# Optimization experiments

Measured on AMD Instinct MI355X. Metric: run time of the kernel, lower is better.

The kernel has to match this reference:

```python
import jax, jax.numpy as jnp
import numpy as np

N_NODES = 50000
N_EDGES = 1600000
NUM_GRAPHS = 512
HID = 128
EDGE_DIM = 64
N_CONV = 4
BN_EPS = 1e-5


def setup_inputs() -> dict:
    key = jax.random.key(0)
    ks = jax.random.split(key, 16)
    x = jax.random.normal(ks[0], (N_NODES, 9), dtype=jnp.float32)
    edge_index = jax.random.randint(ks[1], (2, N_EDGES), 0, N_NODES, dtype=jnp.int64)
    edge_attr = jax.random.normal(ks[2], (N_EDGES, EDGE_DIM), dtype=jnp.float32)
    batch = jnp.sort(jax.random.randint(ks[3], (N_NODES,), 0, NUM_GRAPHS, dtype=jnp.int64))
    s = 0.05
    W_emb = jax.random.normal(ks[4], (9, HID), dtype=jnp.float32) * s
    b_emb = jnp.zeros((HID,), jnp.float32)
    zin = 2 * HID + EDGE_DIM  # 320: cat([x_i, x_j, edge_attr])
    Wf = jax.random.normal(ks[5], (N_CONV, zin, HID), dtype=jnp.float32) * s
    bf = jnp.zeros((N_CONV, HID), jnp.float32)
    Ws = jax.random.normal(ks[6], (N_CONV, zin, HID), dtype=jnp.float32) * s
    bs = jnp.zeros((N_CONV, HID), jnp.float32)
    gamma = jnp.ones((N_CONV, HID), jnp.float32)
    beta = jnp.zeros((N_CONV, HID), jnp.float32)
    W1 = jax.random.normal(ks[7], (HID, HID // 2), dtype=jnp.float32) * s
    b1 = jnp.zeros((HID // 2,), jnp.float32)
    W2 = jax.random.normal(ks[8], (HID // 2, 1), dtype=jnp.float32) * s
    b2 = jnp.zeros((1,), jnp.float32)
    return dict(x=x, edge_index=edge_index, edge_attr=edge_attr, batch=batch,
                W_emb=W_emb, b_emb=b_emb, Wf=Wf, bf=bf, Ws=Ws, bs=bs,
                gamma=gamma, beta=beta, W1=W1, b1=b1, W2=W2, b2=b2)


def _segment_mean(vals, idx, num_segments):
    s = jax.ops.segment_sum(vals, idx, num_segments=num_segments)
    cnt = jax.ops.segment_sum(jnp.ones((vals.shape[0], 1), vals.dtype), idx,
                              num_segments=num_segments)
    return s / jnp.maximum(cnt, 1.0)


def _forward(x, edge_index, edge_attr, batch, W_emb, b_emb, Wf, bf, Ws, bs,
             gamma, beta, W1, b1, W2, b2):
    src, dst = edge_index[0], edge_index[1]  # x_j = x[src], x_i = x[dst]
    h = x @ W_emb + b_emb  # [N, HID]
    for l in range(N_CONV):
        residual = h
        # lin(cat([x_i, x_j, e])) == x_i@W[:H] + x_j@W[H:2H] + e@W[2H:] + b,
        # with node projections done at N granularity before the edge gather.
        f = (h @ Wf[l, :HID])[dst] + (h @ Wf[l, HID:2 * HID])[src] \
            + edge_attr @ Wf[l, 2 * HID:] + bf[l]
        g = (h @ Ws[l, :HID])[dst] + (h @ Ws[l, HID:2 * HID])[src] \
            + edge_attr @ Ws[l, 2 * HID:] + bs[l]
        msg = jax.nn.sigmoid(f) * jax.nn.softplus(g)  # [E, HID]
        aggr = _segment_mean(msg, dst, N_NODES)
        h_conv = aggr + h  # CGConv internal residual
        # BatchNorm1d (training-mode batch stats, biased variance)
        mu = jnp.mean(h_conv, axis=0)
        var = jnp.mean(jnp.square(h_conv - mu), axis=0)
        h_bn = gamma[l] * (h_conv - mu) * jax.lax.rsqrt(var + BN_EPS) + beta[l]
        h = jax.nn.relu(h_bn) + residual  # dropout = identity (eval)
    pooled = _segment_mean(h, batch, NUM_GRAPHS)  # [G, HID]
    out = jax.nn.softplus(pooled @ W1 + b1) @ W2 + b2
    return out.squeeze(-1)  # [G]


def reference(x, edge_index, edge_attr, batch, W_emb, b_emb, Wf, bf, Ws, bs,
              gamma, beta, W1, b1, W2, b2):
    return _forward(x, edge_index, edge_attr, batch, W_emb, b_emb, Wf, bf,
                    Ws, bs, gamma, beta, W1, b1, W2, b2)
```

## Files before the change

kernel.cpp:

```cpp
#include <hip/hip_runtime.h>
#include <math.h>

#define N_NODES 50000
#define N_EDGES 1600000
#define NGRAPH  512
#define HID     128
#define EDIM    64
#define NCONV   4
#define MAXWI   150064
#define NPAD    (N_NODES + 32)
#define EGRID   2560

typedef __attribute__((ext_vector_type(8))) short short8;
typedef __attribute__((ext_vector_type(4))) float f32x4;
typedef unsigned int  u32;
typedef unsigned short u16;

#define MFMA16(a, b, c) __builtin_amdgcn_mfma_f32_16x16x32_bf16(a, b, c, 0, 0, 0)

__device__ __forceinline__ float fsig(float x) {
  return __builtin_amdgcn_rcpf(1.f + __expf(-x));
}
__device__ __forceinline__ float fsp(float x) {
  return fmaxf(x, 0.f) + __logf(1.f + __expf(-fabsf(x)));
}
__device__ __forceinline__ u16 f2bf(float x) {
  u32 u = __float_as_uint(x);
  return (u16)((u + 0x7fff + ((u >> 16) & 1)) >> 16);
}
__device__ __forceinline__ u32 f2bf_pack(float lo, float hi) {
  u32 a = __float_as_uint(lo), b = __float_as_uint(hi);
  u32 ra = (a + 0x7fff + ((a >> 16) & 1)) >> 16;
  u32 rb = (b + 0x7fff + ((b >> 16) & 1)) & 0xffff0000u;
  return ra | rb;
}
__device__ __forceinline__ short8 cvt8(float4 a, float4 b) {
  union { short8 s; u32 u[4]; } r;
  r.u[0] = f2bf_pack(a.x, a.y);
  r.u[1] = f2bf_pack(a.z, a.w);
  r.u[2] = f2bf_pack(b.x, b.y);
  r.u[3] = f2bf_pack(b.z, b.w);
  return r.s;
}

__global__ __launch_bounds__(256) void k_embed(const float* __restrict__ x,
                                               const float* __restrict__ Wemb,
                                               const float* __restrict__ bemb,
                                               float* __restrict__ h,
                                               u16* __restrict__ hb, u16* __restrict__ hlo) {
  int i = blockIdx.x * blockDim.x + threadIdx.x;
  if (i >= N_NODES * HID) return;
  int n = i >> 7, c = i & 127;
  const float* xr = x + (size_t)n * 9;
  float acc = bemb[c];
#pragma unroll
  for (int k = 0; k < 9; k++) acc = fmaf(xr[k], Wemb[k * HID + c], acc);
  h[i] = acc;
  u16 hi16 = f2bf(acc);
  hb[i] = hi16;
  hlo[i] = f2bf(acc - __uint_as_float((u32)hi16 << 16));
}

__global__ __launch_bounds__(256) void k_count(const int* __restrict__ ei, int* __restrict__ cnt) {
  int e = blockIdx.x * blockDim.x + threadIdx.x;
  if (e >= N_EDGES) return;
  atomicAdd(&cnt[ei[N_EDGES + e]], 1);
}

__global__ __launch_bounds__(256) void k_scan1(const int* __restrict__ cnt, int* __restrict__ bsum) {
  __shared__ int s[256];
  int i = blockIdx.x * 256 + threadIdx.x;
  s[threadIdx.x] = (i < N_NODES) ? cnt[i] : 0;
  __syncthreads();
  for (int o = 128; o > 0; o >>= 1) {
    if (threadIdx.x < o) s[threadIdx.x] += s[threadIdx.x + o];
    __syncthreads();
  }
  if (threadIdx.x == 0) bsum[blockIdx.x] = s[0];
}

__global__ __launch_bounds__(256) void k_scan2(int* __restrict__ bsum, int nb) {
  __shared__ int s[256];
  int tid = threadIdx.x;
  s[tid] = (tid < nb) ? bsum[tid] : 0;
  __syncthreads();
  for (int o = 1; o < 256; o <<= 1) {
    int t = (tid >= o) ? s[tid - o] : 0;
    __syncthreads();
    s[tid] += t;
    __syncthreads();
  }
  if (tid < nb) bsum[tid] = (tid == 0) ? 0 : s[tid - 1];
}

__global__ __launch_bounds__(256) void k_scan3(const int* __restrict__ cnt, const int* __restrict__ bsum,
                                               int* __restrict__ row_start, float* __restrict__ inv) {
  __shared__ int s[256];
  int i = blockIdx.x * 256 + threadIdx.x;
  int v = (i < N_NODES) ? cnt[i] : 0;
  s[threadIdx.x] = v;
  __syncthreads();
  for (int o = 1; o < 256; o <<= 1) {
    int t = (threadIdx.x >= o) ? s[threadIdx.x - o] : 0;
    __syncthreads();
    s[threadIdx.x] += t;
    __syncthreads();
  }
  if (i < N_NODES) {
    row_start[i + 1] = s[threadIdx.x] + bsum[blockIdx.x];
    inv[i] = 1.0f / (float)max(v, 1);
    if (i == 0) row_start[0] = 0;
  }
}

__global__ __launch_bounds__(256) void k_fill(const int* __restrict__ ei, const int* __restrict__ row_start,
                                              int* __restrict__ cur, int* __restrict__ eids,
                                              int* __restrict__ esrc) {
  int e = blockIdx.x * blockDim.x + threadIdx.x;
  if (e < 64) {
    eids[N_EDGES + e] = 0;
    esrc[N_EDGES + e] = 0;
  }
  if (e >= N_EDGES) return;
  int s = ei[e], d = ei[N_EDGES + e];
  int pos = row_start[d] + atomicAdd(&cur[d], 1);
  eids[pos] = e;
  esrc[pos] = s;
}

__global__ __launch_bounds__(256) void k_tilecnt(const int* __restrict__ row_start,
                                                 int* __restrict__ tcnt) {
  int i = blockIdx.x * 256 + threadIdx.x;
  if (i >= N_NODES) return;
  tcnt[i] = (row_start[i + 1] - row_start[i] + 15) >> 4;
}

__global__ __launch_bounds__(256) void k_scan3w(const int* __restrict__ tcnt,
                                                const int* __restrict__ bsum,
                                                int* __restrict__ tstart) {
  __shared__ int s[256];
  int i = blockIdx.x * 256 + threadIdx.x;
  int v = (i < N_NODES) ? tcnt[i] : 0;
  s[threadIdx.x] = v;
  __syncthreads();
  for (int o = 1; o < 256; o <<= 1) {
    int t = (threadIdx.x >= o) ? s[threadIdx.x - o] : 0;
    __syncthreads();
    s[threadIdx.x] += t;
    __syncthreads();
  }
  if (i < N_NODES) {
    tstart[i] = s[threadIdx.x] - v + bsum[blockIdx.x];
    if (i == N_NODES - 1) tstart[N_NODES] = s[threadIdx.x] + bsum[blockIdx.x];
  }
}

__global__ __launch_bounds__(256) void k_wfill(const int* __restrict__ row_start,
                                               const int* __restrict__ tstart,
                                               int* __restrict__ wnode, int* __restrict__ wbase) {
  int n = blockIdx.x * 256 + threadIdx.x;
  if (n >= N_NODES) return;
  int rs = row_start[n], re = row_start[n + 1];
  int ts = tstart[n];
  int nt = (re - rs + 15) >> 4;
  for (int mt = 0; mt < nt; ++mt) {
    wnode[ts + mt] = n;
    wbase[ts + mt] = rs + mt * 16;
  }
}

__global__ void k_wpad(const int* __restrict__ tstart,
                       int* __restrict__ wnode, int* __restrict__ wbase) {
  int t = threadIdx.x;
  int nwi = tstart[N_NODES];
  wnode[nwi + t] = 0;
  wbase[nwi + t] = 0;
}

__global__ __launch_bounds__(256) void k_zbound(const int* __restrict__ tstart,
                                                const int* __restrict__ wnode,
                                                float* __restrict__ aggr) {
  int idx = blockIdx.x * 256 + threadIdx.x;
  int seg = idx >> 7, c = idx & 127;
  int b = seg >> 1;
  int NWI = tstart[N_NODES];
  int C = (NWI + EGRID - 1) / EGRID;
  int k0 = b * C;
  if (k0 >= NWI) return;
  int kpos = (seg & 1) ? min(k0 + C - 1, NWI - 1) : k0;
  int node = wnode[kpos];
  aggr[(size_t)node * HID + c] = 0.f;
}

__global__ __launch_bounds__(256) void k_gatherA(const float* __restrict__ eattr,
                                                 const int* __restrict__ eids,
                                                 u16* __restrict__ Ae) {
  int t = blockIdx.x * 256 + threadIdx.x;
  if (t >= (N_EDGES + 64) * 8) return;
  int pos = t >> 3, chunk = t & 7;
  short8* dst = (short8*)((char*)Ae + ((size_t)pos << 7) + (chunk << 4));
  if (pos >= N_EDGES) {
    union { short8 s; u32 u[4]; } z; z.u[0] = z.u[1] = z.u[2] = z.u[3] = 0;
    *dst = z.s;
    return;
  }
  int eid = eids[pos];
  const float* src = eattr + ((size_t)eid << 6) + (chunk << 3);
  float4 a = *(const float4*)src;
  float4 b = *(const float4*)(src + 4);
  *dst = cvt8(a, b);
}

__global__ __launch_bounds__(256) void k_prepW(const float* __restrict__ Wf,
                                               const float* __restrict__ Ws,
                                               u16* __restrict__ Whi, u16* __restrict__ Wlo) {
  int t = blockIdx.x * 256 + threadIdx.x;
  if (t >= 65536 * NCONV) return;
  int l = t >> 16, t16 = t & 65535;
  int c = t16 >> 7, k = t16 & 127;
  int q = c >> 7, col = c & 127;
  const float* W = ((q < 2) ? Wf : Ws) + (size_t)l * 320 * HID;
  int row = (q & 1) ? (128 + k) : k;
  float wv = W[row * HID + col];
  u16 hb16 = f2bf(wv);
  float lo = wv - __uint_as_float((u32)hb16 << 16);
  int nt = (c >> 4) & 7, l15 = c & 15;
  int s = k >> 5, lg = (k >> 3) & 3, i = k & 7;
  int idx = l * 65536 + (((q * 8 + nt) * 4 + s) * 64 + (lg * 16 + l15)) * 8 + i;
  Whi[idx] = hb16;
  Wlo[idx] = f2bf(lo);
}

__global__ __launch_bounds__(256) void k_prepB(const float* __restrict__ Wf,
                                               const float* __restrict__ Ws,
                                               u16* __restrict__ Bhi) {
  int t = blockIdx.x * 256 + threadIdx.x;
  if (t >= 16384 * NCONV) return;
  int l = t >> 14, tid = t & 16383;
  int i = tid & 7, lane = (tid >> 3) & 63, s = (tid >> 9) & 1, nt = tid >> 10;
  int k = s * 32 + ((lane >> 4) << 3) + i;
  int col = ((nt & 7) << 4) + (lane & 15);
  const float* W = ((nt < 8) ? Wf : Ws) + (size_t)l * 320 * HID + 256 * HID;
  Bhi[t] = f2bf(W[k * HID + col]);
}

__global__ __launch_bounds__(256) void k_nodeproj_mfma(
    const u16* __restrict__ hb, const u16* __restrict__ hlo,
    const u16* __restrict__ Whi, const u16* __restrict__ Wlo,
    const float* __restrict__ bf_l, const float* __restrict__ bs_l,
    float* __restrict__ Pd, u32* __restrict__ Ppk) {
  const int lane = threadIdx.x & 63, w = threadIdx.x >> 6;
  const int l15 = lane & 15, lg = lane >> 4;
  const int nb = blockIdx.x * 32;
  const short8* WH = (const short8*)Whi;
  const short8* WL = (const short8*)Wlo;
  f32x4 acc[2][8];
#pragma unroll
  for (int m = 0; m < 2; m++)
#pragma unroll
    for (int nt = 0; nt < 8; nt++) acc[m][nt] = (f32x4){0.f, 0.f, 0.f, 0.f};
  const u32 arow0 = ((u32)(nb + l15)) << 8;
  const u32 arow1 = ((u32)(nb + 16 + l15)) << 8;
#pragma unroll
  for (int s = 0; s < 4; s++) {
    u32 ao0 = arow0 + (s << 6) + (lg << 4);
    u32 ao1 = arow1 + (s << 6) + (lg << 4);
    short8 ah0 = *(const short8*)((const char*)hb + ao0);
    short8 al0 = *(const short8*)((const char*)hlo + ao0);
    short8 ah1 = *(const short8*)((const char*)hb + ao1);
    short8 al1 = *(const short8*)((const char*)hlo + ao1);
#pragma unroll
    for (int nt = 0; nt < 8; nt++) {
      int bi = ((w * 8 + nt) * 4 + s) * 64 + lane;
      short8 bhv = WH[bi];
      short8 blv = WL[bi];
      acc[0][nt] = MFMA16(ah0, bhv, acc[0][nt]);
      acc[0][nt] = MFMA16(ah0, blv, acc[0][nt]);
      acc[0][nt] = MFMA16(al0, bhv, acc[0][nt]);
      acc[1][nt] = MFMA16(ah1, bhv, acc[1][nt]);
      acc[1][nt] = MFMA16(ah1, blv, acc[1][nt]);
      acc[1][nt] = MFMA16(al1, bhv, acc[1][nt]);
    }
  }
  if ((w & 1) == 0) {
    const float* bias = (w == 0) ? bf_l : bs_l;
    int pdoff = (w == 0) ? 0 : 128;
#pragma unroll
    for (int m = 0; m < 2; m++) {
#pragma unroll
      for (int nt = 0; nt < 8; nt++) {
        int col = nt * 16 + l15;
        float b = bias[col];
#pragma unroll
        for (int r = 0; r < 4; r++) {
          int node = nb + m * 16 + lg * 4 + r;
          Pd[(size_t)node * 256 + pdoff + col] = acc[m][nt][r] + b;
        }
      }
    }
  } else {
    int off = (w == 1) ? 0 : 1;
#pragma unroll
    for (int m = 0; m < 2; m++) {
#pragma unroll
      for (int g = 0; g < 4; g++) {
#pragma unroll
        for (int r = 0; r < 4; r++) {
          int node = nb + m * 16 + lg * 4 + r;
          Ppk[(size_t)node * 128 + 2 * (g * 16 + l15) + off] =
              f2bf_pack(acc[m][2 * g][r], acc[m][2 * g + 1][r]);
        }
      }
    }
  }
}

__global__ __launch_bounds__(256, 5) void k_edge_wl(
    const float* __restrict__ Pd, const u32* __restrict__ Ppk,
    const u16* __restrict__ Ae, const int* __restrict__ row_start,
    const int* __restrict__ esrc, const u16* __restrict__ Bhi,
    const int* __restrict__ wnode, const int* __restrict__ wbase,
    const int* __restrict__ tstart, float* __restrict__ aggr) {
  const int tid = threadIdx.x;
  const int lane = tid & 63;
  const int w = tid >> 6;
  const int l15 = lane & 15, lg = lane >> 4;
  const int cb = w * 32;

  const int NWI = tstart[N_NODES];
  int C = (NWI + (int)gridDim.x - 1) / (int)gridDim.x;
  int k0 = (int)blockIdx.x * C;
  int k1 = min(k0 + C, NWI);
  if (k0 >= k1) return;

  const short8* BH = (const short8*)Bhi;
  short8 bh[4][2];
  const int nts[4] = {2 * w, 2 * w + 1, 8 + 2 * w, 9 + 2 * w};
#pragma unroll
  for (int t = 0; t < 4; t++) {
#pragma unroll
    for (int s = 0; s < 2; s++) bh[t][s] = BH[(nts[t] * 2 + s) * 64 + lane];
  }

  const u32 poff = ((u32)(w * 16 + l15)) << 3;
  const int eoff = lg << 2;
  const char* aeb = (const char*)Ae;
  const char* ppb = (const char*)Ppk;

  int wn0 = wnode[k0],     wb0 = wbase[k0];
  int wn1 = wnode[k0 + 1], wb1 = wbase[k0 + 1];
  int wn2 = wnode[k0 + 2], wb2 = wbase[k0 + 2];
  int re0 = row_start[wn0 + 1];
  const float* Pn0 = Pd + (size_t)wn0 * 256;
  float fd0 = Pn0[cb + l15], fd1 = Pn0[cb + 16 + l15];
  float gd0 = Pn0[128 + cb + l15], gd1 = Pn0[128 + cb + 16 + l15];
  uint2 gc0, gc1, gc2, gc3;
  {
    const int* ep0 = esrc + wb0 + eoff;
    int a = ep0[0], b = ep0[1], c2 = ep0[2], d = ep0[3];
    gc0 = *(const uint2*)(ppb + (((u32)a) << 9) + poff);
    gc1 = *(const uint2*)(ppb + (((u32)b) << 9) + poff);
    gc2 = *(const uint2*)(ppb + (((u32)c2) << 9) + poff);
    gc3 = *(const uint2*)(ppb + (((u32)d) << 9) + poff);
  }
  const int* ep1 = esrc + wb1 + eoff;
  int sA0 = ep1[0], sA1 = ep1[1], sA2 = ep1[2], sA3 = ep1[3];
  u32 ab = ((u32)(wb0 + l15) << 7) + ((u32)lg << 4);
  short8 ac0 = *(const short8*)(aeb + ab);
  short8 ac1 = *(const short8*)(aeb + ab + 64);

  float acc0 = 0.f, acc1 = 0.f;
  bool first = true;

  for (int k = k0; k < k1; ++k) {
    uint2 gn0 = *(const uint2*)(ppb + (((u32)sA0) << 9) + poff);
    uint2 gn1 = *(const uint2*)(ppb + (((u32)sA1) << 9) + poff);
    uint2 gn2 = *(const uint2*)(ppb + (((u32)sA2) << 9) + poff);
    uint2 gn3 = *(const uint2*)(ppb + (((u32)sA3) << 9) + poff);
    int wn3 = wnode[k + 3], wb3 = wbase[k + 3];
    const int* ep2 = esrc + wb2 + eoff;
    int t0 = ep2[0], t1 = ep2[1], t2 = ep2[2], t3 = ep2[3];
    int re1 = row_start[wn1 + 1];
    const float* Pn1 = Pd + (size_t)wn1 * 256;
    float nfd0 = Pn1[cb + l15], nfd1 = Pn1[cb + 16 + l15];
    float ngd0 = Pn1[128 + cb + l15], ngd1 = Pn1[128 + cb + 16 + l15];

    f32x4 d0 = {fd0, fd0, fd0, fd0};
    f32x4 d1 = {fd1, fd1, fd1, fd1};
    f32x4 d2 = {gd0, gd0, gd0, gd0};
    f32x4 d3 = {gd1, gd1, gd1, gd1};
    d0 = MFMA16(ac0, bh[0][0], d0); d0 = MFMA16(ac1, bh[0][1], d0);
    d1 = MFMA16(ac0, bh[1][0], d1); d1 = MFMA16(ac1, bh[1][1], d1);
    d2 = MFMA16(ac0, bh[2][0], d2); d2 = MFMA16(ac1, bh[2][1], d2);
    d3 = MFMA16(ac0, bh[3][0], d3); d3 = MFMA16(ac1, bh[3][1], d3);

    u32 ab1 = ((u32)(wb1 + l15) << 7) + ((u32)lg << 4);
    ac0 = *(const short8*)(aeb + ab1);
    ac1 = *(const short8*)(aeb + ab1 + 64);

    const uint2 pgr[4] = {gc0, gc1, gc2, gc3};
    int rowlim = re0 - wb0;
    bool fullt = (rowlim >= 16);
#pragma unroll
    for (int r = 0; r < 4; r++) {
      uint2 pg = pgr[r];
      float f0 = d0[r] + __uint_as_float(pg.x << 16);
      float f1 = d1[r] + __uint_as_float(pg.x & 0xffff0000u);
      float g0 = d2[r] + __uint_as_float(pg.y << 16);
      float g1 = d3[r] + __uint_as_float(pg.y & 0xffff0000u);
      float m0 = fsig(f0) * fsp(g0);
      float m1 = fsig(f1) * fsp(g1);
      if (!fullt) {
        int row = (lg << 2) + r;
        if (row >= rowlim) { m0 = 0.f; m1 = 0.f; }
      }
      acc0 += m0;
      acc1 += m1;
    }

    if (wn0 != wn1 || k == k1 - 1) {
      acc0 += __shfl_xor(acc0, 16); acc0 += __shfl_xor(acc0, 32);
      acc1 += __shfl_xor(acc1, 16); acc1 += __shfl_xor(acc1, 32);
      bool shared = first || (k == k1 - 1);
      if (lane < 16) {
        float* p = &aggr[(size_t)wn0 * HID + cb + lane];
        if (shared) atomicAdd(p, acc0); else *p = acc0;
      } else if (lane < 32) {
        float* p = &aggr[(size_t)wn0 * HID + cb + 16 + l15];
        if (shared) atomicAdd(p, acc1); else *p = acc1;
      }
      acc0 = 0.f; acc1 = 0.f;
      first = false;
    }

    wn0 = wn1; wb0 = wb1; wn1 = wn2; wb1 = wb2; wn2 = wn3; wb2 = wb3;
    re0 = re1;
    fd0 = nfd0; fd1 = nfd1; gd0 = ngd0; gd1 = ngd1;
    gc0 = gn0; gc1 = gn1; gc2 = gn2; gc3 = gn3;
    sA0 = t0; sA1 = t1; sA2 = t2; sA3 = t3;
  }
}

__global__ __launch_bounds__(256) void k_stats(float* __restrict__ hconv,
                                               const float* __restrict__ h,
                                               const float* __restrict__ inv,
                                               float* __restrict__ stats) {
  __shared__ float sb[512];
  int c = threadIdx.x & 127;
  float s1 = 0.f, s2 = 0.f;
  for (int i = blockIdx.x * 256 + threadIdx.x; i < N_NODES * HID; i += gridDim.x * 256) {
    float v = hconv[i] * inv[i >> 7] + h[i];
    hconv[i] = v;
    s1 += v;
    s2 += v * v;
  }
  sb[threadIdx.x] = s1;
  sb[256 + threadIdx.x] = s2;
  __syncthreads();
  if (threadIdx.x < 128) {
    atomicAdd(&stats[c], sb[threadIdx.x] + sb[threadIdx.x + 128]);
    atomicAdd(&stats[128 + c], sb[256 + threadIdx.x] + sb[256 + threadIdx.x + 128]);
  }
}

__global__ __launch_bounds__(256) void k_bn3(const float* __restrict__ hconv, float* __restrict__ h,
                                             const float* __restrict__ stats,
                                             const float* __restrict__ gamma,
                                             const float* __restrict__ beta,
                                             u16* __restrict__ hb, u16* __restrict__ hlo) {
  __shared__ float ssl[256];
  int t = threadIdx.x;
  if (t < 128) {
    float mu = stats[t] * (1.f / N_NODES);
    float var = stats[128 + t] * (1.f / N_NODES) - mu * mu;
    float sc = gamma[t] * rsqrtf(var + 1e-5f);
    ssl[t] = sc;
    ssl[128 + t] = beta[t] - mu * sc;
  }
  __syncthreads();
  int i = blockIdx.x * 256 + t;
  if (i >= N_NODES * HID) return;
  int c = i & 127;
  float v = hconv[i] * ssl[c] + ssl[128 + c];
  float hn = fmaxf(v, 0.f) + h[i];
  h[i] = hn;
  u16 hi16 = f2bf(hn);
  hb[i] = hi16;
  hlo[i] = f2bf(hn - __uint_as_float((u32)hi16 << 16));
}

__global__ __launch_bounds__(128) void k_pool(const float* __restrict__ h, const int* __restrict__ batch,
                                              float* __restrict__ pooled) {
  int g = blockIdx.x;
  int c = threadIdx.x;
  int lo = 0, hi = N_NODES;
  while (lo < hi) { int m = (lo + hi) >> 1; if (batch[m] < g) lo = m + 1; else hi = m; }
  int s = lo;
  lo = 0; hi = N_NODES;
  while (lo < hi) { int m = (lo + hi) >> 1; if (batch[m] < g + 1) lo = m + 1; else hi = m; }
  int e = lo;
  float acc = 0.f;
  for (int n = s; n < e; n++) acc += h[(size_t)n * HID + c];
  pooled[(size_t)g * HID + c] = acc / (float)max(e - s, 1);
}

__global__ __launch_bounds__(64) void k_head(const float* __restrict__ pooled, const float* __restrict__ W1,
                                             const float* __restrict__ b1, const float* __restrict__ W2,
                                             const float* __restrict__ b2, float* __restrict__ out) {
  int g = blockIdx.x;
  int j = threadIdx.x;
  float acc = b1[j];
#pragma unroll 16
  for (int k = 0; k < 128; k++) acc = fmaf(pooled[(size_t)g * HID + k], W1[k * 64 + j], acc);
  float z = fmaxf(acc, 0.f) + __logf(1.f + __expf(-fabsf(acc)));
  float v = z * W2[j];
  for (int o = 32; o > 0; o >>= 1) v += __shfl_down(v, o);
  if (j == 0) out[g] = v + b2[0];
}

extern "C" void kernel_launch(void* const* d_in, const int* in_sizes, int n_in,
                              void* d_out, int out_size, void* d_ws, size_t ws_size,
                              hipStream_t stream) {
  const float* x     = (const float*)d_in[0];
  const int*   ei    = (const int*)d_in[1];
  const float* eattr = (const float*)d_in[2];
  const int*   batch = (const int*)d_in[3];
  const float* Wemb  = (const float*)d_in[4];
  const float* bemb  = (const float*)d_in[5];
  const float* Wf    = (const float*)d_in[6];
  const float* bf    = (const float*)d_in[7];
  const float* Ws    = (const float*)d_in[8];
  const float* bs    = (const float*)d_in[9];
  const float* gamma = (const float*)d_in[10];
  const float* beta  = (const float*)d_in[11];
  const float* W1    = (const float*)d_in[12];
  const float* b1    = (const float*)d_in[13];
  const float* W2    = (const float*)d_in[14];
  const float* b2    = (const float*)d_in[15];
  float* out = (float*)d_out;

  char* ws = (char*)d_ws;
  size_t off = 0;
  auto alloc = [&](size_t bytes) -> char* {
    char* p = ws + off;
    off += (bytes + 255) & ~(size_t)255;
    return p;
  };
  float* h         = (float*)alloc((size_t)N_NODES * HID * 4);
  u16*   hb        = (u16*)alloc((size_t)NPAD * HID * 2);
  u16*   hlo       = (u16*)alloc((size_t)NPAD * HID * 2);
  float* Pd        = (float*)alloc((size_t)NPAD * 256 * 4);
  u32*   Ppk       = (u32*)alloc((size_t)NPAD * 128 * 4);
  float* hconv     = (float*)alloc((size_t)N_NODES * HID * 4);
  int*   row_start = (int*)alloc((size_t)(N_NODES + 1) * 4);
  float* inv       = (float*)alloc((size_t)N_NODES * 4);
  int*   eids      = (int*)alloc((size_t)(N_EDGES + 64) * 4);
  int*   esrc      = (int*)alloc((size_t)(N_EDGES + 64) * 4);
  u16*   Ae        = (u16*)alloc((size_t)(N_EDGES + 64) * EDIM * 2);
  u16*   Bhi       = (u16*)alloc((size_t)16384 * NCONV * 2);
  u16*   Whi       = (u16*)alloc((size_t)65536 * NCONV * 2);
  u16*   Wlo       = (u16*)alloc((size_t)65536 * NCONV * 2);
  int*   tcnt      = (int*)alloc((size_t)N_NODES * 4);
  int*   tstart    = (int*)alloc((size_t)(N_NODES + 1) * 4);
  int*   wnode     = (int*)alloc((size_t)MAXWI * 4);
  int*   wbase     = (int*)alloc((size_t)MAXWI * 4);
  int*   bsum2     = (int*)alloc(256 * 4);
  char*  zbase     = ws + off;
  int*   cnt       = (int*)alloc((size_t)N_NODES * 4);
  int*   cur       = (int*)alloc((size_t)N_NODES * 4);
  float* stats     = (float*)alloc((size_t)NCONV * 256 * 4);
  size_t zbytes    = (size_t)((ws + off) - zbase);
  int*   bsum      = (int*)alloc(256 * 4);
  float* pooled    = (float*)alloc((size_t)NGRAPH * HID * 4);
  (void)ws_size; (void)in_sizes; (void)n_in; (void)out_size;

  hipMemsetAsync(zbase, 0, zbytes, stream);

  k_embed<<<(N_NODES * HID + 255) / 256, 256, 0, stream>>>(x, Wemb, bemb, h, hb, hlo);

  k_count<<<(N_EDGES + 255) / 256, 256, 0, stream>>>(ei, cnt);
  int nb = (N_NODES + 255) / 256;
  k_scan1<<<nb, 256, 0, stream>>>(cnt, bsum);
  k_scan2<<<1, 256, 0, stream>>>(bsum, nb);
  k_scan3<<<nb, 256, 0, stream>>>(cnt, bsum, row_start, inv);
  k_fill<<<(N_EDGES + 255) / 256, 256, 0, stream>>>(ei, row_start, cur, eids, esrc);
  k_gatherA<<<((N_EDGES + 64) * 8 + 255) / 256, 256, 0, stream>>>(eattr, eids, Ae);

  k_tilecnt<<<nb, 256, 0, stream>>>(row_start, tcnt);
  k_scan1<<<nb, 256, 0, stream>>>(tcnt, bsum2);
  k_scan2<<<1, 256, 0, stream>>>(bsum2, nb);
  k_scan3w<<<nb, 256, 0, stream>>>(tcnt, bsum2, tstart);
  k_wfill<<<nb, 256, 0, stream>>>(row_start, tstart, wnode, wbase);
  k_wpad<<<1, 64, 0, stream>>>(tstart, wnode, wbase);

  k_prepW<<<65536 * NCONV / 256, 256, 0, stream>>>(Wf, Ws, Whi, Wlo);
  k_prepB<<<16384 * NCONV / 256, 256, 0, stream>>>(Wf, Ws, Bhi);

  for (int l = 0; l < NCONV; l++) {
    k_nodeproj_mfma<<<(N_NODES + 31) / 32, 256, 0, stream>>>(hb, hlo,
                                                      Whi + l * 65536, Wlo + l * 65536,
                                                      bf + l * HID, bs + l * HID, Pd, Ppk);
    k_zbound<<<(EGRID * 2 * 128 + 255) / 256, 256, 0, stream>>>(tstart, wnode, hconv);
    k_edge_wl<<<EGRID, 256, 0, stream>>>(Pd, Ppk, Ae, row_start, esrc,
                                         Bhi + l * 16384, wnode, wbase, tstart, hconv);
    k_stats<<<2048, 256, 0, stream>>>(hconv, h, inv, stats + l * 256);
    k_bn3<<<(N_NODES * HID + 255) / 256, 256, 0, stream>>>(hconv, h, stats + l * 256,
                                                           gamma + l * HID, beta + l * HID,
                                                           hb, hlo);
  }

  k_pool<<<NGRAPH, HID, 0, stream>>>(h, batch, pooled);
  k_head<<<NGRAPH, 64, 0, stream>>>(pooled, W1, b1, W2, b2, out);
}
```

Baseline: 1.913 ms.

## Pre-scale weights by log2e for native exp2/log2, vectorize stats and BN kernels

Folds the log2(e) factor into the bf16 weight and bias preparation so the edge kernel can call the hardware exp2 and log2 intrinsics directly. The softplus result then comes out in base-2 units and is rescaled by ln2 after the per-node reduction, since sigmoid times softplus is linear in that factor. It also loads edge source indices as int4 and rewrites the stats and BN kernels to use float4 and ushort4 vector accesses with wider per-thread reductions. Prescaling the weights before bf16 rounding slightly changes the rounding error.

After: 2.361 ms. 23.4% more time.

```diff
diff --git a/kernel.cpp b/kernel.cpp
--- a/kernel.cpp
+++ b/kernel.cpp
@@ -10,6 +10,8 @@
 #define MAXWI   150064
 #define NPAD    (N_NODES + 32)
 #define EGRID   2560
+#define LOG2E   1.4426950408889634f
+#define LN2     0.6931471805599453f
 
 typedef __attribute__((ext_vector_type(8))) short short8;
 typedef __attribute__((ext_vector_type(4))) float f32x4;
@@ -18,11 +20,11 @@
 
 #define MFMA16(a, b, c) __builtin_amdgcn_mfma_f32_16x16x32_bf16(a, b, c, 0, 0, 0)
 
-__device__ __forceinline__ float fsig(float x) {
-  return __builtin_amdgcn_rcpf(1.f + __expf(-x));
-}
-__device__ __forceinline__ float fsp(float x) {
-  return fmaxf(x, 0.f) + __logf(1.f + __expf(-fabsf(x)));
+__device__ __forceinline__ float fsig2(float x) {
+  return __builtin_amdgcn_rcpf(1.f + __builtin_amdgcn_exp2f(-x));
+}
+__device__ __forceinline__ float fsp2(float x) {
+  return fmaxf(x, 0.f) + __builtin_amdgcn_logf(1.f + __builtin_amdgcn_exp2f(-fabsf(x)));
 }
 __device__ __forceinline__ u16 f2bf(float x) {
   u32 u = __float_as_uint(x);
@@ -221,7 +223,7 @@
   int q = c >> 7, col = c & 127;
   const float* W = ((q < 2) ? Wf : Ws) + (size_t)l * 320 * HID;
   int row = (q & 1) ? (128 + k) : k;
-  float wv = W[row * HID + col];
+  float wv = W[row * HID + col] * LOG2E;
   u16 hb16 = f2bf(wv);
   float lo = wv - __uint_as_float((u32)hb16 << 16);
   int nt = (c >> 4) & 7, l15 = c & 15;
@@ -241,7 +243,7 @@
   int k = s * 32 + ((lane >> 4) << 3) + i;
   int col = ((nt & 7) << 4) + (lane & 15);
   const float* W = ((nt < 8) ? Wf : Ws) + (size_t)l * 320 * HID + 256 * HID;
-  Bhi[t] = f2bf(W[k * HID + col]);
+  Bhi[t] = f2bf(W[k * HID + col] * LOG2E);
 }
 
 __global__ __launch_bounds__(256) void k_nodeproj_mfma(
@@ -290,7 +292,7 @@
 #pragma unroll
       for (int nt = 0; nt < 8; nt++) {
         int col = nt * 16 + l15;
-        float b = bias[col];
+        float b = bias[col] * LOG2E;
 #pragma unroll
         for (int r = 0; r < 4; r++) {
           int node = nb + m * 16 + lg * 4 + r;
@@ -356,15 +358,13 @@
   float gd0 = Pn0[128 + cb + l15], gd1 = Pn0[128 + cb + 16 + l15];
   uint2 gc0, gc1, gc2, gc3;
   {
-    const int* ep0 = esrc + wb0 + eoff;
-    int a = ep0[0], b = ep0[1], c2 = ep0[2], d = ep0[3];
-    gc0 = *(const uint2*)(ppb + (((u32)a) << 9) + poff);
-    gc1 = *(const uint2*)(ppb + (((u32)b) << 9) + poff);
-    gc2 = *(const uint2*)(ppb + (((u32)c2) << 9) + poff);
-    gc3 = *(const uint2*)(ppb + (((u32)d) << 9) + poff);
-  }
-  const int* ep1 = esrc + wb1 + eoff;
-  int sA0 = ep1[0], sA1 = ep1[1], sA2 = ep1[2], sA3 = ep1[3];
+    int4 sv = *(const int4*)(esrc + wb0 + eoff);
+    gc0 = *(const uint2*)(ppb + (((u32)sv.x) << 9) + poff);
+    gc1 = *(const uint2*)(ppb + (((u32)sv.y) << 9) + poff);
+    gc2 = *(const uint2*)(ppb + (((u32)sv.z) << 9) + poff);
+    gc3 = *(const uint2*)(ppb + (((u32)sv.w) << 9) + poff);
+  }
+  int4 sA = *(const int4*)(esrc + wb1 + eoff);
   u32 ab = ((u32)(wb0 + l15) << 7) + ((u32)lg << 4);
   short8 ac0 = *(const short8*)(aeb + ab);
   short8 ac1 = *(const short8*)(aeb + ab + 64);
@@ -373,13 +373,12 @@
   bool first = true;
 
   for (int k = k0; k < k1; ++k) {
-    uint2 gn0 = *(const uint2*)(ppb + (((u32)sA0) << 9) + poff);
-    uint2 gn1 = *(const uint2*)(ppb + (((u32)sA1) << 9) + poff);
-    uint2 gn2 = *(const uint2*)(ppb + (((u32)sA2) << 9) + poff);
-    uint2 gn3 = *(const uint2*)(ppb + (((u32)sA3) << 9) + poff);
+    uint2 gn0 = *(const uint2*)(ppb + (((u32)sA.x) << 9) + poff);
+    uint2 gn1 = *(const uint2*)(ppb + (((u32)sA.y) << 9) + poff);
+    uint2 gn2 = *(const uint2*)(ppb + (((u32)sA.z) << 9) + poff);
+    uint2 gn3 = *(const uint2*)(ppb + (((u32)sA.w) << 9) + poff);
     int wn3 = wnode[k + 3], wb3 = wbase[k + 3];
-    const int* ep2 = esrc + wb2 + eoff;
-    int t0 = ep2[0], t1 = ep2[1], t2 = ep2[2], t3 = ep2[3];
+    int4 sN = *(const int4*)(esrc + wb2 + eoff);
     int re1 = row_start[wn1 + 1];
     const float* Pn1 = Pd + (size_t)wn1 * 256;
     float nfd0 = Pn1[cb + l15], nfd1 = Pn1[cb + 16 + l15];
@@ -398,18 +397,17 @@
     ac0 = *(const short8*)(aeb + ab1);
     ac1 = *(const short8*)(aeb + ab1 + 64);
 
-    const uint2 pgr[4] = {gc0, gc1, gc2, gc3};
     int rowlim = re0 - wb0;
     bool fullt = (rowlim >= 16);
 #pragma unroll
     for (int r = 0; r < 4; r++) {
-      uint2 pg = pgr[r];
+      uint2 pg = (r == 0) ? gc0 : (r == 1) ? gc1 : (r == 2) ? gc2 : gc3;
       float f0 = d0[r] + __uint_as_float(pg.x << 16);
       float f1 = d1[r] + __uint_as_float(pg.x & 0xffff0000u);
       float g0 = d2[r] + __uint_as_float(pg.y << 16);
       float g1 = d3[r] + __uint_as_float(pg.y & 0xffff0000u);
-      float m0 = fsig(f0) * fsp(g0);
-      float m1 = fsig(f1) * fsp(g1);
+      float m0 = fsig2(f0) * fsp2(g0);
+      float m1 = fsig2(f1) * fsp2(g1);
       if (!fullt) {
         int row = (lg << 2) + r;
         if (row >= rowlim) { m0 = 0.f; m1 = 0.f; }
@@ -421,6 +419,7 @@
     if (wn0 != wn1 || k == k1 - 1) {
       acc0 += __shfl_xor(acc0, 16); acc0 += __shfl_xor(acc0, 32);
       acc1 += __shfl_xor(acc1, 16); acc1 += __shfl_xor(acc1, 32);
+      acc0 *= LN2; acc1 *= LN2;
       bool shared = first || (k == k1 - 1);
       if (lane < 16) {
         float* p = &aggr[(size_t)wn0 * HID + cb + lane];
@@ -437,7 +436,7 @@
     re0 = re1;
     fd0 = nfd0; fd1 = nfd1; gd0 = ngd0; gd1 = ngd1;
     gc0 = gn0; gc1 = gn1; gc2 = gn2; gc3 = gn3;
-    sA0 = t0; sA1 = t1; sA2 = t2; sA3 = t3;
+    sA = sN;
   }
 }
 
@@ -446,20 +445,35 @@
                                                const float* __restrict__ inv,
                                                float* __restrict__ stats) {
   __shared__ float sb[512];
-  int c = threadIdx.x & 127;
-  float s1 = 0.f, s2 = 0.f;
-  for (int i = blockIdx.x * 256 + threadIdx.x; i < N_NODES * HID; i += gridDim.x * 256) {
-    float v = hconv[i] * inv[i >> 7] + h[i];
-    hconv[i] = v;
-    s1 += v;
-    s2 += v * v;
-  }
-  sb[threadIdx.x] = s1;
-  sb[256 + threadIdx.x] = s2;
-  __syncthreads();
-  if (threadIdx.x < 128) {
-    atomicAdd(&stats[c], sb[threadIdx.x] + sb[threadIdx.x + 128]);
-    atomicAdd(&stats[128 + c], sb[256 + threadIdx.x] + sb[256 + threadIdx.x + 128]);
+  int c4 = (threadIdx.x & 31) << 2;
+  float s1[4] = {0.f, 0.f, 0.f, 0.f}, s2[4] = {0.f, 0.f, 0.f, 0.f};
+  const int total4 = N_NODES * HID / 4;
+  for (int i = blockIdx.x * 256 + threadIdx.x; i < total4; i += gridDim.x * 256) {
+    float4 hv = ((const float4*)hconv)[i];
+    float4 rv = ((const float4*)h)[i];
+    float iv = inv[i >> 5];
+    hv.x = hv.x * iv + rv.x; hv.y = hv.y * iv + rv.y;
+    hv.z = hv.z * iv + rv.z; hv.w = hv.w * iv + rv.w;
+    ((float4*)hconv)[i] = hv;
+    s1[0] += hv.x; s1[1] += hv.y; s1[2] += hv.z; s1[3] += hv.w;
+    s2[0] += hv.x * hv.x; s2[1] += hv.y * hv.y; s2[2] += hv.z * hv.z; s2[3] += hv.w * hv.w;
+  }
+#pragma unroll
+  for (int j = 0; j < 4; j++) {
+    sb[threadIdx.x] = s1[j];
+    sb[256 + threadIdx.x] = s2[j];
+    __syncthreads();
+    if (threadIdx.x < 32) {
+      float a1 = 0.f, a2 = 0.f;
+#pragma unroll
+      for (int t = 0; t < 8; t++) {
+        a1 += sb[threadIdx.x + 32 * t];
+        a2 += sb[256 + threadIdx.x + 32 * t];
+      }
+      atomicAdd(&stats[(threadIdx.x << 2) + j], a1);
+      atomicAdd(&stats[128 + (threadIdx.x << 2) + j], a2);
+    }
+    __syncthreads();
   }
 }
 
@@ -479,14 +493,25 @@
   }
   __syncthreads();
   int i = blockIdx.x * 256 + t;
-  if (i >= N_NODES * HID) return;
-  int c = i & 127;
-  float v = hconv[i] * ssl[c] + ssl[128 + c];
-  float hn = fmaxf(v, 0.f) + h[i];
-  h[i] = hn;
-  u16 hi16 = f2bf(hn);
-  hb[i] = hi16;
-  hlo[i] = f2bf(hn - __uint_as_float((u32)hi16 << 16));
+  if (i >= N_NODES * HID / 4) return;
+  int c4 = (i << 2) & 127;
+  float4 hv = ((const float4*)hconv)[i];
+  float4 rv = ((const float4*)h)[i];
+  float4 o;
+  o.x = fmaxf(hv.x * ssl[c4 + 0] + ssl[128 + c4 + 0], 0.f) + rv.x;
+  o.y = fmaxf(hv.y * ssl[c4 + 1] + ssl[128 + c4 + 1], 0.f) + rv.y;
+  o.z = fmaxf(hv.z * ssl[c4 + 2] + ssl[128 + c4 + 2], 0.f) + rv.z;
+  o.w = fmaxf(hv.w * ssl[c4 + 3] + ssl[128 + c4 + 3], 0.f) + rv.w;
+  ((float4*)h)[i] = o;
+  u16 b0 = f2bf(o.x), b1 = f2bf(o.y), b2 = f2bf(o.z), b3 = f2bf(o.w);
+  ushort4 hv4 = {b0, b1, b2, b3};
+  ((ushort4*)hb)[i] = hv4;
+  ushort4 lv4;
+  lv4.x = f2bf(o.x - __uint_as_float((u32)b0 << 16));
+  lv4.y = f2bf(o.y - __uint_as_float((u32)b1 << 16));
+  lv4.z = f2bf(o.z - __uint_as_float((u32)b2 << 16));
+  lv4.w = f2bf(o.w - __uint_as_float((u32)b3 << 16));
+  ((ushort4*)hlo)[i] = lv4;
 }
 
 __global__ __launch_bounds__(128) void k_pool(const float* __restrict__ h, const int* __restrict__ batch,
@@ -604,9 +629,9 @@
     k_edge_wl<<<EGRID, 256, 0, stream>>>(Pd, Ppk, Ae, row_start, esrc,
                                          Bhi + l * 16384, wnode, wbase, tstart, hconv);
     k_stats<<<2048, 256, 0, stream>>>(hconv, h, inv, stats + l * 256);
-    k_bn3<<<(N_NODES * HID + 255) / 256, 256, 0, stream>>>(hconv, h, stats + l * 256,
-                                                           gamma + l * HID, beta + l * HID,
-                                                           hb, hlo);
+    k_bn3<<<(N_NODES * HID / 4 + 255) / 256, 256, 0, stream>>>(hconv, h, stats + l * 256,
+                                                               gamma + l * HID, beta + l * HID,
+                                                               hb, hlo);
   }
 
   k_pool<<<NGRAPH, HID, 0, stream>>>(h, batch, pooled);
```
